# Kernel tuning notes

Hardware: AMD Instinct MI355X
Metric: run time of the kernel (lower is better)

The kernel has to match this reference:

```python
import jax, jax.numpy as jnp
import numpy as np

B, N, D, P, H, DH = 1, 1536, 512, 64, 16, 64
INNER = H * DH  # 1024

def _ln(x, g, b, eps=1e-5):
    m = jnp.mean(x, axis=-1, keepdims=True)
    v = jnp.var(x, axis=-1, keepdims=True)
    return (x - m) / jnp.sqrt(v + eps) * g + b

def setup_inputs() -> dict:
    key = jax.random.key(0)
    ks = jax.random.split(key, 10)
    s = 0.02
    return {
        "node_feats": jax.random.normal(ks[0], (B, N, D), jnp.float32),
        "pair_feats": jax.random.normal(ks[1], (B, N, N, P), jnp.float32),
        "mask": jnp.ones((B, N, N), dtype=bool),
        "ln_node_g": jnp.ones((D,), jnp.float32), "ln_node_b": jnp.zeros((D,), jnp.float32),
        "ln_pair_g": jnp.ones((P,), jnp.float32), "ln_pair_b": jnp.zeros((P,), jnp.float32),
        "Wq": s * jax.random.normal(ks[2], (D, INNER), jnp.float32),
        "bq": jnp.zeros((INNER,), jnp.float32),
        "Wkv": s * jax.random.normal(ks[3], (D, 2 * INNER), jnp.float32),
        "bkv": jnp.zeros((2 * INNER,), jnp.float32),
        "qln_g": jnp.ones((INNER,), jnp.float32), "qln_b": jnp.zeros((INNER,), jnp.float32),
        "kln_g": jnp.ones((INNER,), jnp.float32), "kln_b": jnp.zeros((INNER,), jnp.float32),
        "Wg": s * jax.random.normal(ks[4], (D, INNER), jnp.float32),
        "bg": jnp.zeros((INNER,), jnp.float32),
        "Wbias": s * jax.random.normal(ks[5], (P, H), jnp.float32),
        "Wout": s * jax.random.normal(ks[6], (INNER, D), jnp.float32),
        "bout": jnp.zeros((D,), jnp.float32),
        "n_queries": 0,
        "n_keys": 0,
    }

def reference(node_feats, pair_feats, mask, ln_node_g, ln_node_b, ln_pair_g, ln_pair_b,
              Wq, bq, Wkv, bkv, qln_g, qln_b, kln_g, kln_b, Wg, bg, Wbias, Wout, bout,
              n_queries, n_keys):
    b, n, _ = node_feats.shape
    x = _ln(node_feats, ln_node_g, ln_node_b)          # [b,n,D]
    p = _ln(pair_feats, ln_pair_g, ln_pair_b)          # [b,n,n,P]
    q = _ln(x @ Wq + bq, qln_g, qln_b)                 # [b,n,I]
    kv = x @ Wkv + bkv
    k, v = jnp.split(kv, 2, axis=-1)
    k = _ln(k, kln_g, kln_b)
    g = x @ Wg + bg                                    # gating, [b,n,I]
    bias = jnp.einsum('bijp,ph->bhij', p, Wbias)       # pair bias, [b,h,n,n]
    # split heads -> [b,h,n,dh]
    split = lambda t: t.reshape(b, n, H, DH).transpose(0, 2, 1, 3)
    qh, kh, vh, gh = split(q), split(k), split(v), split(g)
    scale = DH ** -0.5
    sim = jnp.einsum('bhid,bhjd->bhij', qh, kh) * scale
    sim = jnp.where(mask[:, None, :, :], sim, jnp.finfo(sim.dtype).min)
    attn = jax.nn.softmax(sim + bias, axis=-1)
    o = jnp.einsum('bhij,bhjd->bhid', attn, vh)        # [b,h,n,dh]
    o = jax.nn.sigmoid(gh) * o
    o = o.transpose(0, 2, 1, 3).reshape(b, n, INNER)
    return o @ Wout + bout
```

## Files before the change

### kernel.cpp

```cpp
#include <hip/hip_runtime.h>

#define NN 1536
#define DD 512
#define PP 64
#define HH 16
#define DHD 64
#define INNER 1024
#define NCHUNK 4
#define JT_PER 6

typedef __attribute__((ext_vector_type(4))) float f32x4;
typedef __attribute__((ext_vector_type(8))) _Float16 f16x8;
typedef __attribute__((ext_vector_type(4))) _Float16 f16x4;

__device__ inline float wave_sum(float v) {
#pragma unroll
  for (int m = 1; m <= 32; m <<= 1) v += __shfl_xor(v, m);
  return v;
}

__global__ __launch_bounds__(256) void prep_kernel(const float* __restrict__ Wq,
    const float* __restrict__ Wkv, const float* __restrict__ Wg,
    const float* __restrict__ Wout, const float* __restrict__ nf,
    const float* __restrict__ lng, const float* __restrict__ lnb,
    _Float16* __restrict__ BTall, _Float16* __restrict__ WoutT,
    _Float16* __restrict__ x16) {
  int bid = blockIdx.x;
  int tid = threadIdx.x;
  if (bid >= 640) {
    int i = bid - 640;
    int c = tid * 2;
    float2 v = *(const float2*)&nf[(size_t)i * DD + c];
    float s = v.x + v.y, ss = v.x * v.x + v.y * v.y;
    s = wave_sum(s); ss = wave_sum(ss);
    __shared__ float red[2][4];
    int w = tid >> 6;
    if ((tid & 63) == 0) { red[0][w] = s; red[1][w] = ss; }
    __syncthreads();
    s = red[0][0] + red[0][1] + red[0][2] + red[0][3];
    ss = red[1][0] + red[1][1] + red[1][2] + red[1][3];
    float mean = s * (1.f / DD);
    float var = ss * (1.f / DD) - mean * mean;
    float rstd = rsqrtf(var + 1e-5f);
    x16[(size_t)i * DD + c + 0] = (_Float16)((v.x - mean) * rstd * lng[c + 0] + lnb[c + 0]);
    x16[(size_t)i * DD + c + 1] = (_Float16)((v.y - mean) * rstd * lng[c + 1] + lnb[c + 1]);
    return;
  }
  const float* src; int Cs, c0, r0, outStride, outCol; _Float16* dst;
  if (bid < 512) {
    int x = bid & 63, y = bid >> 6;
    int cg0 = x * 64; r0 = y * 64;
    if (cg0 < 1024)      { src = Wq;  Cs = 1024; c0 = cg0; }
    else if (cg0 < 3072) { src = Wkv; Cs = 2048; c0 = cg0 - 1024; }
    else                 { src = Wg;  Cs = 1024; c0 = cg0 - 3072; }
    dst = BTall; outStride = DD; outCol = cg0;
  } else {
    int b = bid - 512;
    int x = b & 7, y = b >> 3;
    c0 = x * 64; r0 = y * 64;
    src = Wout; Cs = DD; dst = WoutT; outStride = INNER; outCol = c0;
  }
  __shared__ float tile[64][65];
  int ri = tid >> 4, ci = (tid & 15) * 4;
#pragma unroll
  for (int p = 0; p < 4; ++p) {
    float4 v = *(const float4*)&src[(size_t)(r0 + ri + p * 16) * Cs + c0 + ci];
    tile[ri + p * 16][ci + 0] = v.x;
    tile[ri + p * 16][ci + 1] = v.y;
    tile[ri + p * 16][ci + 2] = v.z;
    tile[ri + p * 16][ci + 3] = v.w;
  }
  __syncthreads();
  int wr = tid >> 3, wc = (tid & 7) * 8;
#pragma unroll
  for (int p = 0; p < 2; ++p) {
    f16x8 o;
#pragma unroll
    for (int jj = 0; jj < 8; ++jj) o[jj] = (_Float16)tile[wc + jj][wr + p * 32];
    *(f16x8*)&dst[(size_t)(outCol + wr + p * 32) * outStride + r0 + wc] = o;
  }
}

__device__ __forceinline__ void pb_body(int i, int q, int tid,
    const float* __restrict__ pair, const float* __restrict__ pg,
    const float* __restrict__ pb, const float* __restrict__ Wbias,
    _Float16* __restrict__ bias16) {
  int lane = tid & 63, w = tid >> 6;
  int lj = lane & 15, pbase = (lane >> 4) * 8;
  f16x8 wb0, wb1;
#pragma unroll
  for (int jj = 0; jj < 8; ++jj) {
    wb0[jj] = (_Float16)Wbias[(pbase + jj) * HH + lj];
    wb1[jj] = (_Float16)Wbias[(pbase + 32 + jj) * HH + lj];
  }
  float4 g0 = *(const float4*)&pg[pbase],      g1 = *(const float4*)&pg[pbase + 4];
  float4 g2 = *(const float4*)&pg[pbase + 32], g3 = *(const float4*)&pg[pbase + 36];
  float4 b0 = *(const float4*)&pb[pbase],      b1 = *(const float4*)&pb[pbase + 4];
  float4 b2 = *(const float4*)&pb[pbase + 32], b3 = *(const float4*)&pb[pbase + 36];
  __shared__ _Float16 trans[2][16][72];
  int jbase = q * 384 + w * 16 + lj;
  const float* src = &pair[((size_t)i * NN + jbase) * PP];
  float4 v0 = *(const float4*)&src[pbase];
  float4 v1 = *(const float4*)&src[pbase + 4];
  float4 v2 = *(const float4*)&src[pbase + 32];
  float4 v3 = *(const float4*)&src[pbase + 36];
  for (int t = 0; t < 6; ++t) {
    int jt0 = q * 384 + t * 64;
    float4 n0, n1, n2, n3;
    if (t < 5) {
      const float* nsrc = &pair[((size_t)i * NN + jbase + (t + 1) * 64) * PP];
      n0 = *(const float4*)&nsrc[pbase];
      n1 = *(const float4*)&nsrc[pbase + 4];
      n2 = *(const float4*)&nsrc[pbase + 32];
      n3 = *(const float4*)&nsrc[pbase + 36];
    }
    float s = v0.x + v0.y + v0.z + v0.w + v1.x + v1.y + v1.z + v1.w
            + v2.x + v2.y + v2.z + v2.w + v3.x + v3.y + v3.z + v3.w;
    float ss = v0.x * v0.x + v0.y * v0.y + v0.z * v0.z + v0.w * v0.w
             + v1.x * v1.x + v1.y * v1.y + v1.z * v1.z + v1.w * v1.w
             + v2.x * v2.x + v2.y * v2.y + v2.z * v2.z + v2.w * v2.w
             + v3.x * v3.x + v3.y * v3.y + v3.z * v3.z + v3.w * v3.w;
    s += __shfl_xor(s, 16); s += __shfl_xor(s, 32);
    ss += __shfl_xor(ss, 16); ss += __shfl_xor(ss, 32);
    float mean = s * (1.f / PP);
    float var = ss * (1.f / PP) - mean * mean;
    float rstd = rsqrtf(var + 1e-5f);
    f16x8 a0, a1;
    a0[0] = (_Float16)((v0.x - mean) * rstd * g0.x + b0.x);
    a0[1] = (_Float16)((v0.y - mean) * rstd * g0.y + b0.y);
    a0[2] = (_Float16)((v0.z - mean) * rstd * g0.z + b0.z);
    a0[3] = (_Float16)((v0.w - mean) * rstd * g0.w + b0.w);
    a0[4] = (_Float16)((v1.x - mean) * rstd * g1.x + b1.x);
    a0[5] = (_Float16)((v1.y - mean) * rstd * g1.y + b1.y);
    a0[6] = (_Float16)((v1.z - mean) * rstd * g1.z + b1.z);
    a0[7] = (_Float16)((v1.w - mean) * rstd * g1.w + b1.w);
    a1[0] = (_Float16)((v2.x - mean) * rstd * g2.x + b2.x);
    a1[1] = (_Float16)((v2.y - mean) * rstd * g2.y + b2.y);
    a1[2] = (_Float16)((v2.z - mean) * rstd * g2.z + b2.z);
    a1[3] = (_Float16)((v2.w - mean) * rstd * g2.w + b2.w);
    a1[4] = (_Float16)((v3.x - mean) * rstd * g3.x + b3.x);
    a1[5] = (_Float16)((v3.y - mean) * rstd * g3.y + b3.y);
    a1[6] = (_Float16)((v3.z - mean) * rstd * g3.z + b3.z);
    a1[7] = (_Float16)((v3.w - mean) * rstd * g3.w + b3.w);
    f32x4 cacc = {};
    cacc = __builtin_amdgcn_mfma_f32_16x16x32_f16(a0, wb0, cacc, 0, 0, 0);
    cacc = __builtin_amdgcn_mfma_f32_16x16x32_f16(a1, wb1, cacc, 0, 0, 0);
#pragma unroll
    for (int rg = 0; rg < 4; ++rg)
      trans[t & 1][lj][w * 16 + (lane >> 4) * 4 + rg] = (_Float16)cacc[rg];
    __syncthreads();
    int hh = tid >> 4, jc = (tid & 15) * 4;
    f16x4 ov = *(const f16x4*)&trans[t & 1][hh][jc];
    *(f16x4*)&bias16[((size_t)hh * NN + i) * NN + jt0 + jc] = ov;
    v0 = n0; v1 = n1; v2 = n2; v3 = n3;
  }
}

__device__ __forceinline__ void gemm_proj_body(int m0, int n0, int tid,
    const _Float16* __restrict__ A, const _Float16* __restrict__ BT,
    const float* __restrict__ bq, const float* __restrict__ bkv,
    const float* __restrict__ bg, _Float16* __restrict__ C) {
  __shared__ _Float16 As[64][72];
  __shared__ _Float16 Bs[64][72];
  int lane = tid & 63, w = tid >> 6;
  int wm = (w & 1) * 32, wn = (w >> 1) * 32;
  f32x4 acc[2][2] = {};
  int r = tid >> 3, c8 = (tid & 7) * 8;
  int lr = lane & 15, lg = lane >> 4;
  for (int k0 = 0; k0 < DD; k0 += 64) {
    *(f16x8*)&As[r][c8]      = *(const f16x8*)&A[(size_t)(m0 + r) * DD + k0 + c8];
    *(f16x8*)&As[r + 32][c8] = *(const f16x8*)&A[(size_t)(m0 + r + 32) * DD + k0 + c8];
    *(f16x8*)&Bs[r][c8]      = *(const f16x8*)&BT[(size_t)(n0 + r) * DD + k0 + c8];
    *(f16x8*)&Bs[r + 32][c8] = *(const f16x8*)&BT[(size_t)(n0 + r + 32) * DD + k0 + c8];
    __syncthreads();
#pragma unroll
    for (int kf = 0; kf < 2; ++kf) {
      f16x8 a0 = *(const f16x8*)&As[wm + lr][kf * 32 + lg * 8];
      f16x8 a1 = *(const f16x8*)&As[wm + 16 + lr][kf * 32 + lg * 8];
      f16x8 b0 = *(const f16x8*)&Bs[wn + lr][kf * 32 + lg * 8];
      f16x8 b1 = *(const f16x8*)&Bs[wn + 16 + lr][kf * 32 + lg * 8];
      acc[0][0] = __builtin_amdgcn_mfma_f32_16x16x32_f16(a0, b0, acc[0][0], 0, 0, 0);
      acc[0][1] = __builtin_amdgcn_mfma_f32_16x16x32_f16(a0, b1, acc[0][1], 0, 0, 0);
      acc[1][0] = __builtin_amdgcn_mfma_f32_16x16x32_f16(a1, b0, acc[1][0], 0, 0, 0);
      acc[1][1] = __builtin_amdgcn_mfma_f32_16x16x32_f16(a1, b1, acc[1][1], 0, 0, 0);
    }
    __syncthreads();
  }
#pragma unroll
  for (int mi = 0; mi < 2; ++mi)
#pragma unroll
    for (int ni = 0; ni < 2; ++ni)
#pragma unroll
      for (int rg = 0; rg < 4; ++rg) {
        int row = m0 + wm + mi * 16 + lg * 4 + rg;
        int col = n0 + wn + ni * 16 + lr;
        float bv = (col < 1024) ? bq[col] : (col < 3072) ? bkv[col - 1024] : bg[col - 3072];
        C[(size_t)row * 4096 + col] = (_Float16)(acc[mi][ni][rg] + bv);
      }
}

__device__ __forceinline__ void qkv_body(int i, int tid,
    const _Float16* __restrict__ prebuf,
    const float* __restrict__ qg, const float* __restrict__ qb,
    const float* __restrict__ kg, const float* __restrict__ kb,
    _Float16* __restrict__ q16, _Float16* __restrict__ k16) {
  int c = tid * 4;
  const _Float16* rowp = &prebuf[(size_t)i * 4096];
  f16x4 qh = *(const f16x4*)&rowp[c];
  f16x4 kh = *(const f16x4*)&rowp[1024 + c];
  float qv[4], kv[4];
#pragma unroll
  for (int e = 0; e < 4; ++e) { qv[e] = (float)qh[e]; kv[e] = (float)kh[e]; }
  float qs = qv[0] + qv[1] + qv[2] + qv[3];
  float qss = qv[0] * qv[0] + qv[1] * qv[1] + qv[2] * qv[2] + qv[3] * qv[3];
  float ks = kv[0] + kv[1] + kv[2] + kv[3];
  float kss = kv[0] * kv[0] + kv[1] * kv[1] + kv[2] * kv[2] + kv[3] * kv[3];
  qs = wave_sum(qs); qss = wave_sum(qss); ks = wave_sum(ks); kss = wave_sum(kss);
  __shared__ float red[4][4];
  int w = tid >> 6;
  if ((tid & 63) == 0) { red[0][w] = qs; red[1][w] = qss; red[2][w] = ks; red[3][w] = kss; }
  __syncthreads();
  qs = red[0][0] + red[0][1] + red[0][2] + red[0][3];
  qss = red[1][0] + red[1][1] + red[1][2] + red[1][3];
  ks = red[2][0] + red[2][1] + red[2][2] + red[2][3];
  kss = red[3][0] + red[3][1] + red[3][2] + red[3][3];
  float qm = qs * (1.f / INNER), qvr = qss * (1.f / INNER) - qm * qm, qr = rsqrtf(qvr + 1e-5f);
  float km = ks * (1.f / INNER), kvr = kss * (1.f / INNER) - km * km, kr = rsqrtf(kvr + 1e-5f);
  int hh = c >> 6, d = c & 63;
  size_t off = ((size_t)hh * NN + i) * DHD + d;
  f16x4 qo, ko;
#pragma unroll
  for (int e = 0; e < 4; ++e) {
    qo[e] = (_Float16)((qv[e] - qm) * qr * qg[c + e] + qb[c + e]);
    ko[e] = (_Float16)((kv[e] - km) * kr * kg[c + e] + kb[c + e]);
  }
  *(f16x4*)&q16[off] = qo;
  *(f16x4*)&k16[off] = ko;
}

__device__ __forceinline__ void vt_body(int t, int tid,
    const _Float16* __restrict__ prebuf, _Float16* __restrict__ vT16) {
  int z = t / 24, y = t - z * 24;
  __shared__ _Float16 tile[64][72];
  int r0 = y * 64;
  int ri = tid >> 3, ci = (tid & 7) * 8;
#pragma unroll
  for (int p = 0; p < 2; ++p)
    *(f16x8*)&tile[ri + p * 32][ci] =
        *(const f16x8*)&prebuf[(size_t)(r0 + ri + p * 32) * 4096 + 2048 + z * 64 + ci];
  __syncthreads();
#pragma unroll
  for (int p = 0; p < 2; ++p) {
    f16x8 o;
#pragma unroll
    for (int jj = 0; jj < 8; ++jj) o[jj] = tile[ci + jj][ri + p * 32];
    *(f16x8*)&vT16[((size_t)z * DHD + ri + p * 32) * NN + r0 + ci] = o;
  }
}

__device__ __forceinline__ void attn_body(int it, int h, int ck, int tid,
    const _Float16* __restrict__ q16, const _Float16* __restrict__ k16,
    const _Float16* __restrict__ vT16, const _Float16* __restrict__ bias16,
    _Float16* __restrict__ opart, float* __restrict__ mlbuf) {
  int lane = tid & 63, w = tid >> 6;
  int lr = lane & 15, lg = lane >> 4;
  __shared__ _Float16 Kt[64][72];
  __shared__ _Float16 Vt[64][72];
  int ib0 = it * 64;
  int ib = ib0 + w * 16;
  f16x8 qb0 = *(const f16x8*)&q16[((size_t)h * NN + ib + lr) * DHD + lg * 8];
  f16x8 qb1 = *(const f16x8*)&q16[((size_t)h * NN + ib + lr) * DHD + 32 + lg * 8];
  float m = -INFINITY, lsum = 0.f;
  f32x4 oacc[4] = {};
  int sr = tid >> 3, sc = (tid & 7) * 8;
  int jt0g = ck * JT_PER;
  const _Float16* brow = &bias16[((size_t)h * NN + ib + lr) * NN];
  f16x8 kA, kB, vA, vB;
  {
    int j0 = jt0g * 64;
    kA = *(const f16x8*)&k16[((size_t)h * NN + j0 + sr) * DHD + sc];
    kB = *(const f16x8*)&k16[((size_t)h * NN + j0 + sr + 32) * DHD + sc];
    vA = *(const f16x8*)&vT16[((size_t)h * DHD + sr) * NN + j0 + sc];
    vB = *(const f16x8*)&vT16[((size_t)h * DHD + sr + 32) * NN + j0 + sc];
  }
  for (int jj = 0; jj < JT_PER; ++jj) {
    int j0 = (jt0g + jj) * 64;
    *(f16x8*)&Kt[sr][sc] = kA;
    *(f16x8*)&Kt[sr + 32][sc] = kB;
    *(f16x8*)&Vt[sr][sc] = vA;
    *(f16x8*)&Vt[sr + 32][sc] = vB;
    f16x4 bl[4];
#pragma unroll
    for (int jq = 0; jq < 4; ++jq)
      bl[jq] = *(const f16x4*)&brow[j0 + jq * 16 + lg * 4];
    __syncthreads();
    if (jj + 1 < JT_PER) {
      int j1 = j0 + 64;
      kA = *(const f16x8*)&k16[((size_t)h * NN + j1 + sr) * DHD + sc];
      kB = *(const f16x8*)&k16[((size_t)h * NN + j1 + sr + 32) * DHD + sc];
      vA = *(const f16x8*)&vT16[((size_t)h * DHD + sr) * NN + j1 + sc];
      vB = *(const f16x8*)&vT16[((size_t)h * DHD + sr + 32) * NN + j1 + sc];
    }
    float s[4][4];
#pragma unroll
    for (int jq = 0; jq < 4; ++jq) {
      f16x8 ka0 = *(const f16x8*)&Kt[jq * 16 + lr][lg * 8];
      f16x8 ka1 = *(const f16x8*)&Kt[jq * 16 + lr][32 + lg * 8];
      f32x4 c = {};
      c = __builtin_amdgcn_mfma_f32_16x16x32_f16(ka0, qb0, c, 0, 0, 0);
      c = __builtin_amdgcn_mfma_f32_16x16x32_f16(ka1, qb1, c, 0, 0, 0);
#pragma unroll
      for (int r = 0; r < 4; ++r)
        s[jq][r] = c[r] * 0.125f + (float)bl[jq][r];
    }
    float tmax = s[0][0];
#pragma unroll
    for (int jq = 0; jq < 4; ++jq)
#pragma unroll
      for (int r = 0; r < 4; ++r) tmax = fmaxf(tmax, s[jq][r]);
    tmax = fmaxf(tmax, __shfl_xor(tmax, 16));
    tmax = fmaxf(tmax, __shfl_xor(tmax, 32));
    float mn = fmaxf(m, tmax);
    float alpha = __expf(m - mn);
    float ps = 0.f;
    f16x4 pf[4];
#pragma unroll
    for (int jq = 0; jq < 4; ++jq)
#pragma unroll
      for (int r = 0; r < 4; ++r) {
        float p = __expf(s[jq][r] - mn);
        ps += p;
        pf[jq][r] = (_Float16)p;
      }
    ps += __shfl_xor(ps, 16);
    ps += __shfl_xor(ps, 32);
    lsum = lsum * alpha + ps;
    m = mn;
    float ar[4];
#pragma unroll
    for (int r = 0; r < 4; ++r) ar[r] = __shfl(alpha, lg * 4 + r);
#pragma unroll
    for (int dt = 0; dt < 4; ++dt)
#pragma unroll
      for (int r = 0; r < 4; ++r) oacc[dt][r] *= ar[r];
#pragma unroll
    for (int dt = 0; dt < 4; ++dt)
#pragma unroll
      for (int jq = 0; jq < 4; ++jq) {
        f16x4 vb = *(const f16x4*)&Vt[dt * 16 + lr][jq * 16 + lg * 4];
        oacc[dt] = __builtin_amdgcn_mfma_f32_16x16x16f16(pf[jq], vb, oacc[dt], 0, 0, 0);
      }
    __syncthreads();
  }
  size_t pbase = (((size_t)it * HH + h) * NCHUNK + ck) * 4096 + (size_t)w * 1024;
#pragma unroll
  for (int dt = 0; dt < 4; ++dt) {
    f16x4 ov;
#pragma unroll
    for (int r = 0; r < 4; ++r) ov[r] = (_Float16)oacc[dt][r];
    *(f16x4*)&opart[pbase + dt * 256 + lane * 4] = ov;
  }
  if (lg == 0) {
    size_t mb = (((size_t)it * HH + h) * NCHUNK + ck) * 128;
    mlbuf[mb + w * 16 + lr] = m;
    mlbuf[mb + 64 + w * 16 + lr] = lsum;
  }
}

__global__ __launch_bounds__(256) void fat2(const float* __restrict__ pair,
    const float* __restrict__ pg, const float* __restrict__ pb,
    const float* __restrict__ Wbias, _Float16* __restrict__ bias16,
    const _Float16* __restrict__ x16, const _Float16* __restrict__ BTall,
    const float* __restrict__ bq, const float* __restrict__ bkv,
    const float* __restrict__ bg, _Float16* __restrict__ prebuf16) {
  int bid = blockIdx.x;
  int g = bid / 3, r = bid - g * 3;
  int tid = threadIdx.x;
  if (r == 2) {
    gemm_proj_body((g >> 6) * 64, (g & 63) * 64, tid, x16, BTall, bq, bkv, bg, prebuf16);
  } else {
    int p = g * 2 + r;
    pb_body(p % NN, p / NN, tid, pair, pg, pb, Wbias, bias16);
  }
}

__global__ __launch_bounds__(256) void fat3(const float* __restrict__ pair,
    const float* __restrict__ pg, const float* __restrict__ pb,
    const float* __restrict__ Wbias, _Float16* __restrict__ bias16,
    const _Float16* __restrict__ prebuf16,
    const float* __restrict__ qg, const float* __restrict__ qb,
    const float* __restrict__ kg, const float* __restrict__ kb,
    _Float16* __restrict__ q16, _Float16* __restrict__ k16,
    _Float16* __restrict__ vT16) {
  int bid = blockIdx.x;
  int g = bid / 9, r = bid - g * 9;
  int tid = threadIdx.x;
  if (r < 4) {
    pb_body(g * 4 + r, 2, tid, pair, pg, pb, Wbias, bias16);
  } else if (r < 8) {
    qkv_body(g * 4 + (r - 4), tid, prebuf16, qg, qb, kg, kb, q16, k16);
  } else {
    vt_body(g, tid, prebuf16, vT16);
  }
}

__global__ __launch_bounds__(256) void fat4(const float* __restrict__ pair,
    const float* __restrict__ pg, const float* __restrict__ pb,
    const float* __restrict__ Wbias, _Float16* __restrict__ bias16,
    const _Float16* __restrict__ q16, const _Float16* __restrict__ k16,
    const _Float16* __restrict__ vT16, _Float16* __restrict__ opart,
    float* __restrict__ mlbuf) {
  int bid = blockIdx.x;
  int g = bid / 7, r = bid - g * 7;
  int tid = threadIdx.x;
  if (r < 4) {
    pb_body(g * 4 + r, 3, tid, pair, pg, pb, Wbias, bias16);
  } else {
    int a = g * 3 + (r - 4);
    int ck = a % 3, h = (a / 3) % 16, it = a / 48;
    attn_body(it, h, ck, tid, q16, k16, vT16, bias16, opart, mlbuf);
  }
}

__global__ __launch_bounds__(256) void attn_last(const _Float16* __restrict__ q16,
    const _Float16* __restrict__ k16, const _Float16* __restrict__ vT16,
    const _Float16* __restrict__ bias16, _Float16* __restrict__ opart,
    float* __restrict__ mlbuf) {
  attn_body(blockIdx.x, blockIdx.y, 3, threadIdx.x, q16, k16, vT16, bias16, opart, mlbuf);
}

__global__ __launch_bounds__(256) void attn_merge(const _Float16* __restrict__ opart,
    const float* __restrict__ mlbuf, const _Float16* __restrict__ prebuf,
    _Float16* __restrict__ o16) {
  int it = blockIdx.x, h = blockIdx.y;
  int tid = threadIdx.x, lane = tid & 63, w = tid >> 6;
  int lr = lane & 15, lg = lane >> 4;
  __shared__ float sm[NCHUNK][64], sl[NCHUNK][64];
  {
    int c = tid >> 6, i = tid & 63;
    size_t mb = (((size_t)it * HH + h) * NCHUNK + c) * 128;
    sm[c][i] = mlbuf[mb + i];
    sl[c][i] = mlbuf[mb + 64 + i];
  }
  __syncthreads();
  float wc[NCHUNK][4], linv[4];
#pragma unroll
  for (int r = 0; r < 4; ++r) {
    int i_loc = w * 16 + lg * 4 + r;
    float mg = sm[0][i_loc];
#pragma unroll
    for (int c = 1; c < NCHUNK; ++c) mg = fmaxf(mg, sm[c][i_loc]);
    float lt = 0.f;
#pragma unroll
    for (int c = 0; c < NCHUNK; ++c) {
      float e = __expf(sm[c][i_loc] - mg);
      wc[c][r] = e;
      lt += e * sl[c][i_loc];
    }
    linv[r] = 1.f / lt;
  }
  size_t base = ((size_t)it * HH + h) * NCHUNK * 4096 + (size_t)w * 1024;
#pragma unroll
  for (int dt = 0; dt < 4; ++dt) {
    float o[4] = {};
#pragma unroll
    for (int c = 0; c < NCHUNK; ++c) {
      f16x4 v = *(const f16x4*)&opart[base + (size_t)c * 4096 + dt * 256 + lane * 4];
#pragma unroll
      for (int r = 0; r < 4; ++r) o[r] += wc[c][r] * (float)v[r];
    }
    int d = dt * 16 + lr;
#pragma unroll
    for (int r = 0; r < 4; ++r) {
      int i = it * 64 + w * 16 + lg * 4 + r;
      float gt = (float)prebuf[(size_t)i * 4096 + 3072 + h * DHD + d];
      float val = o[r] * linv[r] * (1.f / (1.f + __expf(-gt)));
      o16[(size_t)i * INNER + h * DHD + d] = (_Float16)val;
    }
  }
}

__global__ __launch_bounds__(256) void gemm_f16(const _Float16* __restrict__ A,
    const _Float16* __restrict__ BT, const float* __restrict__ bias,
    float* __restrict__ C, int M, int N, int K) {
  __shared__ _Float16 As[64][72];
  __shared__ _Float16 Bs[64][72];
  int tid = threadIdx.x, lane = tid & 63, w = tid >> 6;
  int m0 = blockIdx.y * 64, n0 = blockIdx.x * 64;
  int wm = (w & 1) * 32, wn = (w >> 1) * 32;
  f32x4 acc[2][2] = {};
  int r = tid >> 3, c8 = (tid & 7) * 8;
  int lr = lane & 15, lg = lane >> 4;
  for (int k0 = 0; k0 < K; k0 += 64) {
    *(f16x8*)&As[r][c8]      = *(const f16x8*)&A[(size_t)(m0 + r) * K + k0 + c8];
    *(f16x8*)&As[r + 32][c8] = *(const f16x8*)&A[(size_t)(m0 + r + 32) * K + k0 + c8];
    *(f16x8*)&Bs[r][c8]      = *(const f16x8*)&BT[(size_t)(n0 + r) * K + k0 + c8];
    *(f16x8*)&Bs[r + 32][c8] = *(const f16x8*)&BT[(size_t)(n0 + r + 32) * K + k0 + c8];
    __syncthreads();
#pragma unroll
    for (int kf = 0; kf < 2; ++kf) {
      f16x8 a0 = *(const f16x8*)&As[wm + lr][kf * 32 + lg * 8];
      f16x8 a1 = *(const f16x8*)&As[wm + 16 + lr][kf * 32 + lg * 8];
      f16x8 b0 = *(const f16x8*)&Bs[wn + lr][kf * 32 + lg * 8];
      f16x8 b1 = *(const f16x8*)&Bs[wn + 16 + lr][kf * 32 + lg * 8];
      acc[0][0] = __builtin_amdgcn_mfma_f32_16x16x32_f16(a0, b0, acc[0][0], 0, 0, 0);
      acc[0][1] = __builtin_amdgcn_mfma_f32_16x16x32_f16(a0, b1, acc[0][1], 0, 0, 0);
      acc[1][0] = __builtin_amdgcn_mfma_f32_16x16x32_f16(a1, b0, acc[1][0], 0, 0, 0);
      acc[1][1] = __builtin_amdgcn_mfma_f32_16x16x32_f16(a1, b1, acc[1][1], 0, 0, 0);
    }
    __syncthreads();
  }
#pragma unroll
  for (int mi = 0; mi < 2; ++mi)
#pragma unroll
    for (int ni = 0; ni < 2; ++ni)
#pragma unroll
      for (int rg = 0; rg < 4; ++rg) {
        int row = m0 + wm + mi * 16 + lg * 4 + rg;
        int col = n0 + wn + ni * 16 + lr;
        C[(size_t)row * N + col] = acc[mi][ni][rg] + bias[col];
      }
}

extern "C" void kernel_launch(void* const* d_in, const int* in_sizes, int n_in,
                              void* d_out, int out_size, void* d_ws, size_t ws_size,
                              hipStream_t stream) {
  const float* node  = (const float*)d_in[0];
  const float* pair  = (const float*)d_in[1];
  const float* ln_ng = (const float*)d_in[3];
  const float* ln_nb = (const float*)d_in[4];
  const float* ln_pg = (const float*)d_in[5];
  const float* ln_pb = (const float*)d_in[6];
  const float* Wq    = (const float*)d_in[7];
  const float* bq    = (const float*)d_in[8];
  const float* Wkv   = (const float*)d_in[9];
  const float* bkv   = (const float*)d_in[10];
  const float* qlg   = (const float*)d_in[11];
  const float* qlb   = (const float*)d_in[12];
  const float* klg   = (const float*)d_in[13];
  const float* klb   = (const float*)d_in[14];
  const float* Wg    = (const float*)d_in[15];
  const float* bg    = (const float*)d_in[16];
  const float* Wbias = (const float*)d_in[17];
  const float* Wout  = (const float*)d_in[18];
  const float* bout  = (const float*)d_in[19];
  float* out = (float*)d_out;

  char* ws = (char*)d_ws;
  const size_t MB = 1u << 20;
  _Float16* BTall    = (_Float16*)(ws + 0 * MB);
  _Float16* WoutT    = (_Float16*)(ws + 4 * MB);
  _Float16* x16      = (_Float16*)(ws + 5 * MB);
  _Float16* prebuf16 = (_Float16*)(ws + 8 * MB);
  _Float16* q16      = (_Float16*)(ws + 20 * MB);
  _Float16* k16      = (_Float16*)(ws + 23 * MB);
  _Float16* vT16     = (_Float16*)(ws + 29 * MB);
  _Float16* o16      = (_Float16*)(ws + 32 * MB);
  _Float16* bias16   = (_Float16*)(ws + 36 * MB);
  _Float16* opart    = (_Float16*)(ws + 112 * MB);
  float*    mlbuf    = (float*)(ws + 126 * MB);

  prep_kernel<<<640 + NN, 256, 0, stream>>>(Wq, Wkv, Wg, Wout, node, ln_ng, ln_nb,
                                            BTall, WoutT, x16);
  fat2<<<4608, 256, 0, stream>>>(pair, ln_pg, ln_pb, Wbias, bias16,
                                 x16, BTall, bq, bkv, bg, prebuf16);
  fat3<<<3456, 256, 0, stream>>>(pair, ln_pg, ln_pb, Wbias, bias16,
                                 prebuf16, qlg, qlb, klg, klb, q16, k16, vT16);
  fat4<<<2688, 256, 0, stream>>>(pair, ln_pg, ln_pb, Wbias, bias16,
                                 q16, k16, vT16, opart, mlbuf);
  attn_last<<<dim3(NN / 64, HH), 256, 0, stream>>>(q16, k16, vT16, bias16, opart, mlbuf);
  attn_merge<<<dim3(NN / 64, HH), 256, 0, stream>>>(opart, mlbuf, prebuf16, o16);
  gemm_f16<<<dim3(DD / 64, NN / 64), 256, 0, stream>>>(o16, WoutT, bout, out, NN, DD, INNER);
}
```

Measured before the change: 240.9 us.

## Fuse last attention chunk with merge kernel and use nontemporal pair loads

The final attention chunk now runs in the same kernel as the chunk merge. Its output accumulator and softmax stats stay in registers, so they are no longer written to opart and mlbuf and read back, and one kernel launch goes away. Per-row merge weights are computed per lane and broadcast with shuffles instead of staged through shared memory. The pair-bias loads of the large pair tensor now use nontemporal hints to avoid polluting the cache. The fused kernel may need more registers, which could lower occupancy.

```diff
diff --git a/kernel.cpp b/kernel.cpp
--- a/kernel.cpp
+++ b/kernel.cpp
@@ -87,61 +87,53 @@
     _Float16* __restrict__ bias16) {
   int lane = tid & 63, w = tid >> 6;
   int lj = lane & 15, pbase = (lane >> 4) * 8;
+  const int off0 = 0, off1 = 4, off2 = 32, off3 = 36;
   f16x8 wb0, wb1;
 #pragma unroll
   for (int jj = 0; jj < 8; ++jj) {
     wb0[jj] = (_Float16)Wbias[(pbase + jj) * HH + lj];
     wb1[jj] = (_Float16)Wbias[(pbase + 32 + jj) * HH + lj];
   }
-  float4 g0 = *(const float4*)&pg[pbase],      g1 = *(const float4*)&pg[pbase + 4];
-  float4 g2 = *(const float4*)&pg[pbase + 32], g3 = *(const float4*)&pg[pbase + 36];
-  float4 b0 = *(const float4*)&pb[pbase],      b1 = *(const float4*)&pb[pbase + 4];
-  float4 b2 = *(const float4*)&pb[pbase + 32], b3 = *(const float4*)&pb[pbase + 36];
+  f32x4 gv0 = *(const f32x4*)&pg[pbase + off0], gv1 = *(const f32x4*)&pg[pbase + off1];
+  f32x4 gv2 = *(const f32x4*)&pg[pbase + off2], gv3 = *(const f32x4*)&pg[pbase + off3];
+  f32x4 bb0 = *(const f32x4*)&pb[pbase + off0], bb1 = *(const f32x4*)&pb[pbase + off1];
+  f32x4 bb2 = *(const f32x4*)&pb[pbase + off2], bb3 = *(const f32x4*)&pb[pbase + off3];
   __shared__ _Float16 trans[2][16][72];
   int jbase = q * 384 + w * 16 + lj;
-  const float* src = &pair[((size_t)i * NN + jbase) * PP];
-  float4 v0 = *(const float4*)&src[pbase];
-  float4 v1 = *(const float4*)&src[pbase + 4];
-  float4 v2 = *(const float4*)&src[pbase + 32];
-  float4 v3 = *(const float4*)&src[pbase + 36];
+  const float* srcp = &pair[((size_t)i * NN + jbase) * PP];
+  f32x4 v0 = __builtin_nontemporal_load((const f32x4*)&srcp[pbase + off0]);
+  f32x4 v1 = __builtin_nontemporal_load((const f32x4*)&srcp[pbase + off1]);
+  f32x4 v2 = __builtin_nontemporal_load((const f32x4*)&srcp[pbase + off2]);
+  f32x4 v3 = __builtin_nontemporal_load((const f32x4*)&srcp[pbase + off3]);
   for (int t = 0; t < 6; ++t) {
     int jt0 = q * 384 + t * 64;
-    float4 n0, n1, n2, n3;
+    f32x4 n0, n1, n2, n3;
     if (t < 5) {
-      const float* nsrc = &pair[((size_t)i * NN + jbase + (t + 1) * 64) * PP];
-      n0 = *(const float4*)&nsrc[pbase];
-      n1 = *(const float4*)&nsrc[pbase + 4];
-      n2 = *(const float4*)&nsrc[pbase + 32];
-      n3 = *(const float4*)&nsrc[pbase + 36];
-    }
-    float s = v0.x + v0.y + v0.z + v0.w + v1.x + v1.y + v1.z + v1.w
-            + v2.x + v2.y + v2.z + v2.w + v3.x + v3.y + v3.z + v3.w;
-    float ss = v0.x * v0.x + v0.y * v0.y + v0.z * v0.z + v0.w * v0.w
-             + v1.x * v1.x + v1.y * v1.y + v1.z * v1.z + v1.w * v1.w
-             + v2.x * v2.x + v2.y * v2.y + v2.z * v2.z + v2.w * v2.w
-             + v3.x * v3.x + v3.y * v3.y + v3.z * v3.z + v3.w * v3.w;
+      const float* ns = &pair[((size_t)i * NN + jbase + (t + 1) * 64) * PP];
+      n0 = __builtin_nontemporal_load((const f32x4*)&ns[pbase + off0]);
+      n1 = __builtin_nontemporal_load((const f32x4*)&ns[pbase + off1]);
+      n2 = __builtin_nontemporal_load((const f32x4*)&ns[pbase + off2]);
+      n3 = __builtin_nontemporal_load((const f32x4*)&ns[pbase + off3]);
+    }
+    float s = 0.f, ss = 0.f;
+#pragma unroll
+    for (int e = 0; e < 4; ++e) {
+      s += v0[e] + v1[e] + v2[e] + v3[e];
+      ss += v0[e] * v0[e] + v1[e] * v1[e] + v2[e] * v2[e] + v3[e] * v3[e];
+    }
     s += __shfl_xor(s, 16); s += __shfl_xor(s, 32);
     ss += __shfl_xor(ss, 16); ss += __shfl_xor(ss, 32);
     float mean = s * (1.f / PP);
     float var = ss * (1.f / PP) - mean * mean;
     float rstd = rsqrtf(var + 1e-5f);
     f16x8 a0, a1;
-    a0[0] = (_Float16)((v0.x - mean) * rstd * g0.x + b0.x);
-    a0[1] = (_Float16)((v0.y - mean) * rstd * g0.y + b0.y);
-    a0[2] = (_Float16)((v0.z - mean) * rstd * g0.z + b0.z);
-    a0[3] = (_Float16)((v0.w - mean) * rstd * g0.w + b0.w);
-    a0[4] = (_Float16)((v1.x - mean) * rstd * g1.x + b1.x);
-    a0[5] = (_Float16)((v1.y - mean) * rstd * g1.y + b1.y);
-    a0[6] = (_Float16)((v1.z - mean) * rstd * g1.z + b1.z);
-    a0[7] = (_Float16)((v1.w - mean) * rstd * g1.w + b1.w);
-    a1[0] = (_Float16)((v2.x - mean) * rstd * g2.x + b2.x);
-    a1[1] = (_Float16)((v2.y - mean) * rstd * g2.y + b2.y);
-    a1[2] = (_Float16)((v2.z - mean) * rstd * g2.z + b2.z);
-    a1[3] = (_Float16)((v2.w - mean) * rstd * g2.w + b2.w);
-    a1[4] = (_Float16)((v3.x - mean) * rstd * g3.x + b3.x);
-    a1[5] = (_Float16)((v3.y - mean) * rstd * g3.y + b3.y);
-    a1[6] = (_Float16)((v3.z - mean) * rstd * g3.z + b3.z);
-    a1[7] = (_Float16)((v3.w - mean) * rstd * g3.w + b3.w);
+#pragma unroll
+    for (int e = 0; e < 4; ++e) {
+      a0[e]     = (_Float16)((v0[e] - mean) * rstd * gv0[e] + bb0[e]);
+      a0[4 + e] = (_Float16)((v1[e] - mean) * rstd * gv1[e] + bb1[e]);
+      a1[e]     = (_Float16)((v2[e] - mean) * rstd * gv2[e] + bb2[e]);
+      a1[4 + e] = (_Float16)((v3[e] - mean) * rstd * gv3[e] + bb3[e]);
+    }
     f32x4 cacc = {};
     cacc = __builtin_amdgcn_mfma_f32_16x16x32_f16(a0, wb0, cacc, 0, 0, 0);
     cacc = __builtin_amdgcn_mfma_f32_16x16x32_f16(a1, wb1, cacc, 0, 0, 0);
@@ -227,15 +219,15 @@
   float qm = qs * (1.f / INNER), qvr = qss * (1.f / INNER) - qm * qm, qr = rsqrtf(qvr + 1e-5f);
   float km = ks * (1.f / INNER), kvr = kss * (1.f / INNER) - km * km, kr = rsqrtf(kvr + 1e-5f);
   int hh = c >> 6, d = c & 63;
-  size_t off = ((size_t)hh * NN + i) * DHD + d;
+  size_t offo = ((size_t)hh * NN + i) * DHD + d;
   f16x4 qo, ko;
 #pragma unroll
   for (int e = 0; e < 4; ++e) {
     qo[e] = (_Float16)((qv[e] - qm) * qr * qg[c + e] + qb[c + e]);
     ko[e] = (_Float16)((kv[e] - km) * kr * kg[c + e] + kb[c + e]);
   }
-  *(f16x4*)&q16[off] = qo;
-  *(f16x4*)&k16[off] = ko;
+  *(f16x4*)&q16[offo] = qo;
+  *(f16x4*)&k16[offo] = ko;
 }
 
 __device__ __forceinline__ void vt_body(int t, int tid,
@@ -258,10 +250,10 @@
   }
 }
 
-__device__ __forceinline__ void attn_body(int it, int h, int ck, int tid,
+__device__ __forceinline__ void attn_core(int it, int h, int ck, int tid,
     const _Float16* __restrict__ q16, const _Float16* __restrict__ k16,
     const _Float16* __restrict__ vT16, const _Float16* __restrict__ bias16,
-    _Float16* __restrict__ opart, float* __restrict__ mlbuf) {
+    f32x4 oacc[4], float& mOut, float& lOut) {
   int lane = tid & 63, w = tid >> 6;
   int lr = lane & 15, lg = lane >> 4;
   __shared__ _Float16 Kt[64][72];
@@ -271,7 +263,6 @@
   f16x8 qb0 = *(const f16x8*)&q16[((size_t)h * NN + ib + lr) * DHD + lg * 8];
   f16x8 qb1 = *(const f16x8*)&q16[((size_t)h * NN + ib + lr) * DHD + 32 + lg * 8];
   float m = -INFINITY, lsum = 0.f;
-  f32x4 oacc[4] = {};
   int sr = tid >> 3, sc = (tid & 7) * 8;
   int jt0g = ck * JT_PER;
   const _Float16* brow = &bias16[((size_t)h * NN + ib + lr) * NN];
@@ -352,6 +343,19 @@
       }
     __syncthreads();
   }
+  mOut = m;
+  lOut = lsum;
+}
+
+__device__ __forceinline__ void attn_body(int it, int h, int ck, int tid,
+    const _Float16* __restrict__ q16, const _Float16* __restrict__ k16,
+    const _Float16* __restrict__ vT16, const _Float16* __restrict__ bias16,
+    _Float16* __restrict__ opart, float* __restrict__ mlbuf) {
+  int lane = tid & 63, w = tid >> 6;
+  int lr = lane & 15, lg = lane >> 4;
+  f32x4 oacc[4] = {};
+  float m, lsum;
+  attn_core(it, h, ck, tid, q16, k16, vT16, bias16, oacc, m, lsum);
   size_t pbase = (((size_t)it * HH + h) * NCHUNK + ck) * 4096 + (size_t)w * 1024;
 #pragma unroll
   for (int dt = 0; dt < 4; ++dt) {
@@ -422,59 +426,57 @@
   }
 }
 
-__global__ __launch_bounds__(256) void attn_last(const _Float16* __restrict__ q16,
+__global__ __launch_bounds__(256) void attn_final(const _Float16* __restrict__ q16,
     const _Float16* __restrict__ k16, const _Float16* __restrict__ vT16,
-    const _Float16* __restrict__ bias16, _Float16* __restrict__ opart,
-    float* __restrict__ mlbuf) {
-  attn_body(blockIdx.x, blockIdx.y, 3, threadIdx.x, q16, k16, vT16, bias16, opart, mlbuf);
-}
-
-__global__ __launch_bounds__(256) void attn_merge(const _Float16* __restrict__ opart,
+    const _Float16* __restrict__ bias16, const _Float16* __restrict__ opart,
     const float* __restrict__ mlbuf, const _Float16* __restrict__ prebuf,
     _Float16* __restrict__ o16) {
   int it = blockIdx.x, h = blockIdx.y;
   int tid = threadIdx.x, lane = tid & 63, w = tid >> 6;
   int lr = lane & 15, lg = lane >> 4;
-  __shared__ float sm[NCHUNK][64], sl[NCHUNK][64];
-  {
-    int c = tid >> 6, i = tid & 63;
+  f32x4 oacc[4] = {};
+  float m3, l3;
+  attn_core(it, h, 3, tid, q16, k16, vT16, bias16, oacc, m3, l3);
+  float mc[NCHUNK], lc[NCHUNK];
+#pragma unroll
+  for (int c = 0; c < 3; ++c) {
     size_t mb = (((size_t)it * HH + h) * NCHUNK + c) * 128;
-    sm[c][i] = mlbuf[mb + i];
-    sl[c][i] = mlbuf[mb + 64 + i];
-  }
-  __syncthreads();
-  float wc[NCHUNK][4], linv[4];
+    mc[c] = mlbuf[mb + w * 16 + lr];
+    lc[c] = mlbuf[mb + 64 + w * 16 + lr];
+  }
+  mc[3] = m3; lc[3] = l3;
+  float mg = fmaxf(fmaxf(mc[0], mc[1]), fmaxf(mc[2], mc[3]));
+  float wcc[NCHUNK], lt = 0.f;
+#pragma unroll
+  for (int c = 0; c < NCHUNK; ++c) {
+    wcc[c] = __expf(mc[c] - mg);
+    lt += wcc[c] * lc[c];
+  }
+  float wq[NCHUNK][4], ltq[4];
 #pragma unroll
   for (int r = 0; r < 4; ++r) {
-    int i_loc = w * 16 + lg * 4 + r;
-    float mg = sm[0][i_loc];
-#pragma unroll
-    for (int c = 1; c < NCHUNK; ++c) mg = fmaxf(mg, sm[c][i_loc]);
-    float lt = 0.f;
-#pragma unroll
-    for (int c = 0; c < NCHUNK; ++c) {
-      float e = __expf(sm[c][i_loc] - mg);
-      wc[c][r] = e;
-      lt += e * sl[c][i_loc];
-    }
-    linv[r] = 1.f / lt;
-  }
-  size_t base = ((size_t)it * HH + h) * NCHUNK * 4096 + (size_t)w * 1024;
+    ltq[r] = __shfl(lt, lg * 4 + r);
+#pragma unroll
+    for (int c = 0; c < NCHUNK; ++c) wq[c][r] = __shfl(wcc[c], lg * 4 + r);
+  }
 #pragma unroll
   for (int dt = 0; dt < 4; ++dt) {
-    float o[4] = {};
-#pragma unroll
-    for (int c = 0; c < NCHUNK; ++c) {
-      f16x4 v = *(const f16x4*)&opart[base + (size_t)c * 4096 + dt * 256 + lane * 4];
-#pragma unroll
-      for (int r = 0; r < 4; ++r) o[r] += wc[c][r] * (float)v[r];
+    float o[4];
+#pragma unroll
+    for (int r = 0; r < 4; ++r) o[r] = wq[3][r] * oacc[dt][r];
+#pragma unroll
+    for (int c = 0; c < 3; ++c) {
+      size_t base = (((size_t)it * HH + h) * NCHUNK + c) * 4096 + (size_t)w * 1024;
+      f16x4 v = *(const f16x4*)&opart[base + dt * 256 + lane * 4];
+#pragma unroll
+      for (int r = 0; r < 4; ++r) o[r] += wq[c][r] * (float)v[r];
     }
     int d = dt * 16 + lr;
 #pragma unroll
     for (int r = 0; r < 4; ++r) {
       int i = it * 64 + w * 16 + lg * 4 + r;
       float gt = (float)prebuf[(size_t)i * 4096 + 3072 + h * DHD + d];
-      float val = o[r] * linv[r] * (1.f / (1.f + __expf(-gt)));
+      float val = o[r] / ltq[r] * (1.f / (1.f + __expf(-gt)));
       o16[(size_t)i * INNER + h * DHD + d] = (_Float16)val;
     }
   }
@@ -568,7 +570,7 @@
                                  prebuf16, qlg, qlb, klg, klb, q16, k16, vT16);
   fat4<<<2688, 256, 0, stream>>>(pair, ln_pg, ln_pb, Wbias, bias16,
                                  q16, k16, vT16, opart, mlbuf);
-  attn_last<<<dim3(NN / 64, HH), 256, 0, stream>>>(q16, k16, vT16, bias16, opart, mlbuf);
-  attn_merge<<<dim3(NN / 64, HH), 256, 0, stream>>>(opart, mlbuf, prebuf16, o16);
+  attn_final<<<dim3(NN / 64, HH), 256, 0, stream>>>(q16, k16, vT16, bias16,
+                                                    opart, mlbuf, prebuf16, o16);
   gemm_f16<<<dim3(DD / 64, NN / 64), 256, 0, stream>>>(o16, WoutT, bout, out, NN, DD, INNER);
 }
```

New measurement: 245.6 us. No clear change (+2.0%).
